# Kernel tuning notes

Hardware: AMD Instinct MI355X
Metric: run time of the kernel (lower is better)

The kernel has to match this reference:

```python
import jax, jax.numpy as jnp
import numpy as np

B, S, D_IN, D_OUT, H = 2, 2048, 1024, 1024, 16
HD = D_OUT // H  # head dim = 64


def setup_inputs() -> dict:
    key = jax.random.key(0)
    ks = jax.random.split(key, 9)
    s_in = 1.0 / np.sqrt(D_IN)
    s_out = 1.0 / np.sqrt(D_OUT)
    return {
        "X": jax.random.normal(ks[0], (B, S, D_IN), dtype=jnp.float32),
        "Wq": jax.random.uniform(ks[1], (D_OUT, D_IN), jnp.float32, -s_in, s_in),
        "bq": jax.random.uniform(ks[2], (D_OUT,), jnp.float32, -s_in, s_in),
        "Wk": jax.random.uniform(ks[3], (D_OUT, D_IN), jnp.float32, -s_in, s_in),
        "bk": jax.random.uniform(ks[4], (D_OUT,), jnp.float32, -s_in, s_in),
        "Wv": jax.random.uniform(ks[5], (D_OUT, D_IN), jnp.float32, -s_in, s_in),
        "bv": jax.random.uniform(ks[6], (D_OUT,), jnp.float32, -s_in, s_in),
        "Wo": jax.random.uniform(ks[7], (D_OUT, D_OUT), jnp.float32, -s_out, s_out),
        "bo": jax.random.uniform(ks[8], (D_OUT,), jnp.float32, -s_out, s_out),
    }


def reference(X, Wq, bq, Wk, bk, Wv, bv, Wo, bo):
    scale = jnp.asarray(HD ** 0.5, X.dtype)  # self.dim = sqrt(head_dim)
    q = X @ Wq.T + bq  # [B,S,D_OUT]
    k = X @ Wk.T + bk
    v = X @ Wv.T + bv
    # split heads: b s (h d) -> b h s d
    q = q.reshape(B, S, H, HD).transpose(0, 2, 1, 3)
    k = k.reshape(B, S, H, HD).transpose(0, 2, 1, 3)
    v = v.reshape(B, S, H, HD).transpose(0, 2, 1, 3)
    scores = jnp.einsum('bhsd,bhtd->bhst', q, k) / scale  # [B,H,S,S]
    causal = jnp.triu(jnp.ones((S, S), dtype=bool), k=1)
    scores = jnp.where(causal, -jnp.inf, scores)
    weights = jax.nn.softmax(scores, axis=-1)
    out = jnp.einsum('bhst,bhtd->bhsd', weights, v)  # [B,H,S,HD]
    out = out.transpose(0, 2, 1, 3).reshape(B, S, D_OUT)  # b h s d -> b s (h d)
    return out @ Wo.T + bo
```

## Files before the change

kernel.cpp:

```cpp
#include <hip/hip_runtime.h>
#include <hip/hip_bf16.h>

typedef __bf16 bf16_t;
typedef __bf16 bf16x8 __attribute__((ext_vector_type(8)));
typedef float  f32x4  __attribute__((ext_vector_type(4)));
typedef unsigned short ushort_t;

#define MFMA16(a, b, c) __builtin_amdgcn_mfma_f32_16x16x32_bf16((a), (b), (c), 0, 0, 0)
#define GLDS16(g, l) __builtin_amdgcn_global_load_lds( \
    (const __attribute__((address_space(1))) unsigned int*)(g), \
    (__attribute__((address_space(3))) unsigned int*)(l), 16, 0, 0)

#define WAITCNT_VM(n)  (0x0F70 | (n))
#define WAITCNT_LGKM0  0xC07F


__global__ __launch_bounds__(64) void sniff_kernel(const ushort_t* __restrict__ x,
                                                   int* __restrict__ flag)
{
    const int t = threadIdx.x;
    const ushort_t u = x[2 * t];
    const int e = (u >> 7) & 0xFF;
    const unsigned long long m = __ballot(e >= 0xA0);
    if (t == 0) *flag = (m != 0ull) ? 1 : 0;
}

__global__ __launch_bounds__(256) void cvt_all(
    const void* __restrict__ X,  const void* __restrict__ W0, const void* __restrict__ W1,
    const void* __restrict__ W2, const void* __restrict__ W3,
    bf16_t* __restrict__ Xb, bf16_t* __restrict__ Wb, const int* __restrict__ flag)
{
    const long long i = (long long)(blockIdx.x * 256 + threadIdx.x) * 8;
    const void* src;
    bf16_t* dst;
    long long off;
    if (i < 4194304) { src = X; dst = Xb; off = i; }
    else {
        const int w = (int)((i - 4194304) >> 20);
        off = (i - 4194304) & 1048575;
        src = (w == 0) ? W0 : (w == 1) ? W1 : (w == 2) ? W2 : W3;
        dst = Wb + (size_t)w * 1048576;
    }
    if (*flag) {
        const float* s = (const float*)src + off;
        const float4 a = *(const float4*)(s);
        const float4 b = *(const float4*)(s + 4);
        bf16x8 o;
        o[0] = (bf16_t)a.x; o[1] = (bf16_t)a.y; o[2] = (bf16_t)a.z; o[3] = (bf16_t)a.w;
        o[4] = (bf16_t)b.x; o[5] = (bf16_t)b.y; o[6] = (bf16_t)b.z; o[7] = (bf16_t)b.w;
        *(bf16x8*)(dst + off) = o;
    } else {
        *(bf16x8*)(dst + off) = *(const bf16x8*)((const bf16_t*)src + off);
    }
}

__global__ __launch_bounds__(256) void cvt_bias(const void* __restrict__ b0, const void* __restrict__ b1,
                                                const void* __restrict__ b2, const void* __restrict__ b3,
                                                float* __restrict__ dst, const int* __restrict__ flag)
{
    const int t = blockIdx.x * 256 + threadIdx.x;
    if (*flag) {
        dst[t]        = ((const float*)b0)[t];
        dst[1024 + t] = ((const float*)b1)[t];
        dst[2048 + t] = ((const float*)b2)[t];
        dst[3072 + t] = ((const float*)b3)[t];
    } else {
        dst[t]        = (float)((const bf16_t*)b0)[t];
        dst[1024 + t] = (float)((const bf16_t*)b1)[t];
        dst[2048 + t] = (float)((const bf16_t*)b2)[t];
        dst[3072 + t] = (float)((const bf16_t*)b3)[t];
    }
}

template<int TM>
__global__ __launch_bounds__(256, 2) void gemm_nt(
    const bf16_t* __restrict__ A,
    const bf16_t* __restrict__ W0, const bf16_t* __restrict__ W1, const bf16_t* __restrict__ W2,
    const float* __restrict__ b0, const float* __restrict__ b1, const float* __restrict__ b2,
    void* __restrict__ C, int ldc, const int* __restrict__ flag, int is_out)
{
    constexpr int MI = TM / 32;
    constexpr int G  = (TM == 128) ? 4 : 3;
    __shared__ bf16_t Ash[3][TM * 32];
    __shared__ bf16_t Bsh[3][128 * 32];

    const int f32out = is_out ? *flag : 0;

    const int tid  = threadIdx.x;
    const int wid  = tid >> 6;
    const int lane = tid & 63;
    const int g    = lane >> 4;
    const int c    = lane & 15;

    const int m0  = blockIdx.x * TM;
    const int n0  = blockIdx.y * 128;
    const int mat = n0 >> 10;
    const bf16_t* W  = (mat == 0) ? W0 : (mat == 1) ? W1 : W2;
    const float*  bs = (mat == 0) ? b0 : (mat == 1) ? b1 : b2;
    const int nw = n0 & 1023;

    const int srow = lane >> 2;
    const int sblk = (lane & 3) ^ ((lane >> 3) & 3);
    const bf16_t* Ag = A + (size_t)(m0 + wid * (TM / 4) + srow) * 1024 + sblk * 8;
    const bf16_t* Wg = W + (size_t)(nw + wid * 32 + srow) * 1024 + sblk * 8;

    const int waveM = (wid >> 1) * (TM / 2);
    const int waveN = (wid & 1) * 64;

    f32x4 acc[MI][4] = {};
    const int fblk = (g ^ ((c >> 1) & 3)) * 8;

    auto stage = [&](int t, int buf) {
        const int k0 = t * 32;
        bf16_t* As = &Ash[buf][(wid * (TM / 4)) * 32];
        bf16_t* Bs = &Bsh[buf][(wid * 32) * 32];
        GLDS16(Ag + k0, As);
        if (TM == 128) GLDS16(Ag + (size_t)16 * 1024 + k0, As + 16 * 32);
        GLDS16(Wg + k0, Bs);
        GLDS16(Wg + (size_t)16 * 1024 + k0, Bs + 16 * 32);
    };

    stage(0, 0);
    stage(1, 1);

    #pragma unroll 3
    for (int k = 0; k < 32; ++k) {
        if (k < 30) {
            stage(k + 2, (k + 2) % 3);
            __builtin_amdgcn_s_waitcnt(WAITCNT_VM(2 * G));
        } else if (k == 30) {
            __builtin_amdgcn_s_waitcnt(WAITCNT_VM(G));
        } else {
            __builtin_amdgcn_s_waitcnt(WAITCNT_VM(0));
        }
        __builtin_amdgcn_s_barrier();
        asm volatile("" ::: "memory");

        const int cur = k % 3;
        bf16x8 af[MI], bfr[4];
        #pragma unroll
        for (int i = 0; i < MI; ++i)
            af[i] = *(const bf16x8*)(&Ash[cur][(waveM + i * 16 + c) * 32 + fblk]);
        #pragma unroll
        for (int j = 0; j < 4; ++j)
            bfr[j] = *(const bf16x8*)(&Bsh[cur][(waveN + j * 16 + c) * 32 + fblk]);
        #pragma unroll
        for (int i = 0; i < MI; ++i)
            #pragma unroll
            for (int j = 0; j < 4; ++j)
                acc[i][j] = MFMA16(af[i], bfr[j], acc[i][j]);

        asm volatile("" ::: "memory");
        __builtin_amdgcn_s_waitcnt(WAITCNT_LGKM0);
        __builtin_amdgcn_s_barrier();
    }

    #pragma unroll
    for (int j = 0; j < 4; ++j) {
        const int col = n0 + waveN + j * 16 + c;
        const float bv = bs[col & 1023];
        #pragma unroll
        for (int i = 0; i < MI; ++i) {
            const int row = m0 + waveM + i * 16 + g * 4;
            #pragma unroll
            for (int r = 0; r < 4; ++r) {
                const float val = acc[i][j][r] + bv;
                const size_t idx = (size_t)(row + r) * ldc + col;
                if (f32out) ((float*)C)[idx] = val;
                else        ((bf16_t*)C)[idx] = (bf16_t)val;
            }
        }
    }
}

__global__ __launch_bounds__(256) void transpose_v(
    const bf16_t* __restrict__ QKV, bf16_t* __restrict__ Vt)
{
    __shared__ ushort_t T[64][72];
    const int tid = threadIdx.x;
    const int r   = tid >> 2;
    const int c0  = (tid & 3) * 16;
    const int bh  = blockIdx.y;
    const int b   = bh >> 4, h = bh & 15;
    const int s0  = blockIdx.x * 64;

    const ushort_t* src = (const ushort_t*)QKV +
        (size_t)(b * 2048 + s0 + r) * 3072 + 2048 + h * 64 + c0;
    ushort_t v[16];
    *(uint4*)(&v[0]) = *(const uint4*)(src);
    *(uint4*)(&v[8]) = *(const uint4*)(src + 8);
    #pragma unroll
    for (int i = 0; i < 16; ++i) T[c0 + i][r] = v[i];
    __syncthreads();
    ushort_t* dst = (ushort_t*)Vt + ((size_t)bh * 64 + r) * 2048 + s0 + c0;
    *(uint4*)(dst)     = *(const uint4*)(&T[r][c0]);
    *(uint4*)(dst + 8) = *(const uint4*)(&T[r][c0 + 8]);
}

__global__ __launch_bounds__(256, 2) void attn_kernel(
    const bf16_t* __restrict__ QKV, const bf16_t* __restrict__ Vt,
    bf16_t* __restrict__ O)
{
    __shared__ bf16_t Ksh[64][72];
    __shared__ bf16_t Vsh[64][72];
    __shared__ bf16_t Psh[4][32][72];

    const int tid  = threadIdx.x;
    const int wid  = tid >> 6;
    const int lane = tid & 63;
    const int g    = lane >> 4;
    const int c    = lane & 15;

    const int bh = blockIdx.y;
    const int b  = bh >> 4, h = bh & 15;
    const int qt = (bh < 16) ? blockIdx.x : (15 - blockIdx.x);
    const int q0 = qt * 128;
    const int nt = 2 * qt + 2;

    bf16x8 aq[2][2];
    #pragma unroll
    for (int qf = 0; qf < 2; ++qf) {
        const bf16_t* qp = QKV + (size_t)(b * 2048 + q0 + wid * 32 + qf * 16 + c) * 3072 + h * 64;
        #pragma unroll
        for (int kb = 0; kb < 2; ++kb) {
            bf16x8 t = *(const bf16x8*)(qp + kb * 32 + g * 8);
            #pragma unroll
            for (int j = 0; j < 8; ++j) t[j] = (bf16_t)((float)t[j] * 0.125f);
            aq[qf][kb] = t;
        }
    }

    float li[2][4] = {};
    f32x4 o[2][4]  = {};

    const int sr  = tid >> 2;
    const int sc0 = (tid & 3) * 16;
    const bf16_t* Kg = QKV + (size_t)(b * 2048 + sr) * 3072 + 1024 + h * 64 + sc0;
    const bf16_t* Vg = Vt + ((size_t)bh * 64 + sr) * 2048 + sc0;

    uint4 kr0 = *(const uint4*)(Kg);
    uint4 kr1 = *(const uint4*)(Kg + 8);
    uint4 vr0 = *(const uint4*)(Vg);
    uint4 vr1 = *(const uint4*)(Vg + 8);

    for (int jt = 0; jt < nt; ++jt) {
        *(uint4*)(&Ksh[sr][sc0])     = kr0;
        *(uint4*)(&Ksh[sr][sc0 + 8]) = kr1;
        *(uint4*)(&Vsh[sr][sc0])     = vr0;
        *(uint4*)(&Vsh[sr][sc0 + 8]) = vr1;
        __syncthreads();

        if (jt + 1 < nt) {
            const size_t ko = (size_t)(jt + 1) * 64 * 3072;
            kr0 = *(const uint4*)(Kg + ko);
            kr1 = *(const uint4*)(Kg + ko + 8);
            vr0 = *(const uint4*)(Vg + (jt + 1) * 64);
            vr1 = *(const uint4*)(Vg + (jt + 1) * 64 + 8);
        }

        f32x4 s[2][4] = {};
        #pragma unroll
        for (int n = 0; n < 4; ++n)
            #pragma unroll
            for (int kb = 0; kb < 2; ++kb) {
                const bf16x8 kf = *(const bf16x8*)(&Ksh[n * 16 + c][kb * 32 + g * 8]);
                s[0][n] = MFMA16(aq[0][kb], kf, s[0][n]);
                s[1][n] = MFMA16(aq[1][kb], kf, s[1][n]);
            }

        if (jt >= nt - 2) {
            const int j0 = jt * 64;
            #pragma unroll
            for (int qf = 0; qf < 2; ++qf) {
                const int qrow = q0 + wid * 32 + qf * 16 + g * 4;
                #pragma unroll
                for (int n = 0; n < 4; ++n)
                    #pragma unroll
                    for (int r = 0; r < 4; ++r)
                        if (j0 + n * 16 + c > qrow + r) s[qf][n][r] = -1e30f;
            }
        }

        #pragma unroll
        for (int qf = 0; qf < 2; ++qf)
            #pragma unroll
            for (int n = 0; n < 4; ++n)
                #pragma unroll
                for (int r = 0; r < 4; ++r) {
                    const float p = __expf(s[qf][n][r]);
                    li[qf][r] += p;
                    Psh[wid][qf * 16 + g * 4 + r][n * 16 + c] = (bf16_t)p;
                }
        __builtin_amdgcn_wave_barrier();

        #pragma unroll
        for (int kb = 0; kb < 2; ++kb) {
            const bf16x8 ap0 = *(const bf16x8*)(&Psh[wid][c][kb * 32 + g * 8]);
            const bf16x8 ap1 = *(const bf16x8*)(&Psh[wid][16 + c][kb * 32 + g * 8]);
            #pragma unroll
            for (int d = 0; d < 4; ++d) {
                const bf16x8 vf = *(const bf16x8*)(&Vsh[d * 16 + c][kb * 32 + g * 8]);
                o[0][d] = MFMA16(ap0, vf, o[0][d]);
                o[1][d] = MFMA16(ap1, vf, o[1][d]);
            }
        }
        __syncthreads();
    }

    #pragma unroll
    for (int off = 1; off < 16; off <<= 1)
        #pragma unroll
        for (int qf = 0; qf < 2; ++qf)
            #pragma unroll
            for (int r = 0; r < 4; ++r)
                li[qf][r] += __shfl_xor(li[qf][r], off, 64);

    #pragma unroll
    for (int qf = 0; qf < 2; ++qf) {
        const int orow = b * 2048 + q0 + wid * 32 + qf * 16 + g * 4;
        #pragma unroll
        for (int r = 0; r < 4; ++r) {
            const float inv = 1.0f / li[qf][r];
            #pragma unroll
            for (int d = 0; d < 4; ++d)
                O[(size_t)(orow + r) * 1024 + h * 64 + d * 16 + c] = (bf16_t)(o[qf][d][r] * inv);
        }
    }
}

extern "C" void kernel_launch(void* const* d_in, const int* in_sizes, int n_in,
                              void* d_out, int out_size, void* d_ws, size_t ws_size,
                              hipStream_t stream)
{
    const void* X  = d_in[0];
    const void* Wq = d_in[1];  const void* bq = d_in[2];
    const void* Wk = d_in[3];  const void* bk = d_in[4];
    const void* Wv = d_in[5];  const void* bv = d_in[6];
    const void* Wo = d_in[7];  const void* bo = d_in[8];

    int*    flag  = (int*)d_ws;
    float*  biasF = (float*)((char*)d_ws + 16);
    bf16_t* Xb    = (bf16_t*)((char*)d_ws + 16 + 16384);
    bf16_t* Wb    = Xb  + (size_t)4096 * 1024;
    bf16_t* QKV   = Wb  + (size_t)4 * 1024 * 1024;
    bf16_t* Vt    = QKV + (size_t)4096 * 3072;
    bf16_t* Ao    = Vt  + (size_t)4096 * 1024;

    const size_t MW = (size_t)1024 * 1024;

    sniff_kernel<<<1, 64, 0, stream>>>((const ushort_t*)X, flag);
    cvt_all<<<4096, 256, 0, stream>>>(X, Wq, Wk, Wv, Wo, Xb, Wb, flag);
    cvt_bias<<<4, 256, 0, stream>>>(bq, bk, bv, bo, biasF, flag);

    gemm_nt<128><<<dim3(32, 24), 256, 0, stream>>>(
        Xb, Wb, Wb + MW, Wb + 2 * MW,
        biasF, biasF + 1024, biasF + 2048, QKV, 3072, flag, 0);
    transpose_v<<<dim3(32, 32), 256, 0, stream>>>(QKV, Vt);
    attn_kernel<<<dim3(16, 32), 256, 0, stream>>>(QKV, Vt, Ao);
    gemm_nt<64><<<dim3(64, 8), 256, 0, stream>>>(
        Ao, Wb + 3 * MW, Wb + 3 * MW, Wb + 3 * MW,
        biasF + 3072, biasF + 3072, biasF + 3072, d_out, 1024, flag, 1);
}
```

Before: 216.8 us.

## Fuse dtype sniff and bias conversion into cvt_all, write V transposed from GEMM

Drops the separate sniff and bias-conversion kernels: every cvt_all block now detects the input dtype itself with a ballot and two extra blocks convert the biases. Removes the transpose_v kernel by having the QKV GEMM write V directly in head-transposed layout from its epilogue. Also switches the QKV GEMM from 128-row to 64-row tiles, which doubles the block count. Together this cuts three launches and a full V round trip through memory, at the cost of strided 8-byte stores in the V epilogue and less reuse per tile in the GEMM.

Measured after the change: 226.1 us. +4.3%, slower.

```diff
diff --git a/kernel.cpp b/kernel.cpp
--- a/kernel.cpp
+++ b/kernel.cpp
@@ -15,22 +15,34 @@
 #define WAITCNT_LGKM0  0xC07F
 
 
-__global__ __launch_bounds__(64) void sniff_kernel(const ushort_t* __restrict__ x,
-                                                   int* __restrict__ flag)
-{
-    const int t = threadIdx.x;
-    const ushort_t u = x[2 * t];
-    const int e = (u >> 7) & 0xFF;
-    const unsigned long long m = __ballot(e >= 0xA0);
-    if (t == 0) *flag = (m != 0ull) ? 1 : 0;
-}
-
 __global__ __launch_bounds__(256) void cvt_all(
     const void* __restrict__ X,  const void* __restrict__ W0, const void* __restrict__ W1,
     const void* __restrict__ W2, const void* __restrict__ W3,
-    bf16_t* __restrict__ Xb, bf16_t* __restrict__ Wb, const int* __restrict__ flag)
+    const void* __restrict__ c0, const void* __restrict__ c1,
+    const void* __restrict__ c2, const void* __restrict__ c3,
+    bf16_t* __restrict__ Xb, bf16_t* __restrict__ Wb, float* __restrict__ biasF,
+    int* __restrict__ flag)
 {
-    const long long i = (long long)(blockIdx.x * 256 + threadIdx.x) * 8;
+    const int tid  = threadIdx.x;
+    const int lane = tid & 63;
+    const ushort_t u = ((const ushort_t*)X)[2 * lane];
+    const int e = (u >> 7) & 0xFF;
+    const int f = (__ballot(e >= 0xA0) != 0ull) ? 1 : 0;
+
+    const int bid = blockIdx.x;
+    if (bid >= 4096) {
+        if (bid == 4096 && tid == 0) *flag = f;
+        const int idx = ((bid - 4096) * 256 + tid) * 8;
+        const int w = idx >> 10, off = idx & 1023;
+        const void* src = (w == 0) ? c0 : (w == 1) ? c1 : (w == 2) ? c2 : c3;
+        #pragma unroll
+        for (int r = 0; r < 8; ++r)
+            biasF[idx + r] = f ? ((const float*)src)[off + r]
+                               : (float)((const bf16_t*)src)[off + r];
+        return;
+    }
+
+    const long long i = (long long)bid * 2048 + tid * 8;
     const void* src;
     bf16_t* dst;
     long long off;
@@ -41,7 +53,7 @@
         src = (w == 0) ? W0 : (w == 1) ? W1 : (w == 2) ? W2 : W3;
         dst = Wb + (size_t)w * 1048576;
     }
-    if (*flag) {
+    if (f) {
         const float* s = (const float*)src + off;
         const float4 a = *(const float4*)(s);
         const float4 b = *(const float4*)(s + 4);
@@ -54,30 +66,13 @@
     }
 }
 
-__global__ __launch_bounds__(256) void cvt_bias(const void* __restrict__ b0, const void* __restrict__ b1,
-                                                const void* __restrict__ b2, const void* __restrict__ b3,
-                                                float* __restrict__ dst, const int* __restrict__ flag)
-{
-    const int t = blockIdx.x * 256 + threadIdx.x;
-    if (*flag) {
-        dst[t]        = ((const float*)b0)[t];
-        dst[1024 + t] = ((const float*)b1)[t];
-        dst[2048 + t] = ((const float*)b2)[t];
-        dst[3072 + t] = ((const float*)b3)[t];
-    } else {
-        dst[t]        = (float)((const bf16_t*)b0)[t];
-        dst[1024 + t] = (float)((const bf16_t*)b1)[t];
-        dst[2048 + t] = (float)((const bf16_t*)b2)[t];
-        dst[3072 + t] = (float)((const bf16_t*)b3)[t];
-    }
-}
-
 template<int TM>
 __global__ __launch_bounds__(256, 2) void gemm_nt(
     const bf16_t* __restrict__ A,
     const bf16_t* __restrict__ W0, const bf16_t* __restrict__ W1, const bf16_t* __restrict__ W2,
     const float* __restrict__ b0, const float* __restrict__ b1, const float* __restrict__ b2,
-    void* __restrict__ C, int ldc, const int* __restrict__ flag, int is_out)
+    void* __restrict__ C, int ldc, bf16_t* __restrict__ Vt, int fuse_vt,
+    const int* __restrict__ flag, int is_out)
 {
     constexpr int MI = TM / 32;
     constexpr int G  = (TM == 128) ? 4 : 3;
@@ -155,6 +150,26 @@
         __builtin_amdgcn_s_barrier();
     }
 
+    if (fuse_vt && mat == 2) {
+        #pragma unroll
+        for (int j = 0; j < 4; ++j) {
+            const int col  = n0 + waveN + j * 16 + c;
+            const int hcol = col & 1023;
+            const float bv = bs[hcol];
+            const int h = hcol >> 6, d = hcol & 63;
+            #pragma unroll
+            for (int i = 0; i < MI; ++i) {
+                const int row = m0 + waveM + i * 16 + g * 4;
+                const int bb = row >> 11, s = row & 2047;
+                bf16_t pk[4];
+                #pragma unroll
+                for (int r = 0; r < 4; ++r) pk[r] = (bf16_t)(acc[i][j][r] + bv);
+                *(uint2*)(&Vt[(((size_t)bb * 16 + h) * 64 + d) * 2048 + s]) = *(uint2*)pk;
+            }
+        }
+        return;
+    }
+
     #pragma unroll
     for (int j = 0; j < 4; ++j) {
         const int col = n0 + waveN + j * 16 + c;
@@ -171,30 +186,6 @@
             }
         }
     }
-}
-
-__global__ __launch_bounds__(256) void transpose_v(
-    const bf16_t* __restrict__ QKV, bf16_t* __restrict__ Vt)
-{
-    __shared__ ushort_t T[64][72];
-    const int tid = threadIdx.x;
-    const int r   = tid >> 2;
-    const int c0  = (tid & 3) * 16;
-    const int bh  = blockIdx.y;
-    const int b   = bh >> 4, h = bh & 15;
-    const int s0  = blockIdx.x * 64;
-
-    const ushort_t* src = (const ushort_t*)QKV +
-        (size_t)(b * 2048 + s0 + r) * 3072 + 2048 + h * 64 + c0;
-    ushort_t v[16];
-    *(uint4*)(&v[0]) = *(const uint4*)(src);
-    *(uint4*)(&v[8]) = *(const uint4*)(src + 8);
-    #pragma unroll
-    for (int i = 0; i < 16; ++i) T[c0 + i][r] = v[i];
-    __syncthreads();
-    ushort_t* dst = (ushort_t*)Vt + ((size_t)bh * 64 + r) * 2048 + s0 + c0;
-    *(uint4*)(dst)     = *(const uint4*)(&T[r][c0]);
-    *(uint4*)(dst + 8) = *(const uint4*)(&T[r][c0 + 8]);
 }
 
 __global__ __launch_bounds__(256, 2) void attn_kernel(
@@ -348,16 +339,14 @@
 
     const size_t MW = (size_t)1024 * 1024;
 
-    sniff_kernel<<<1, 64, 0, stream>>>((const ushort_t*)X, flag);
-    cvt_all<<<4096, 256, 0, stream>>>(X, Wq, Wk, Wv, Wo, Xb, Wb, flag);
-    cvt_bias<<<4, 256, 0, stream>>>(bq, bk, bv, bo, biasF, flag);
-
-    gemm_nt<128><<<dim3(32, 24), 256, 0, stream>>>(
+    cvt_all<<<4098, 256, 0, stream>>>(X, Wq, Wk, Wv, Wo, bq, bk, bv, bo,
+                                      Xb, Wb, biasF, flag);
+
+    gemm_nt<64><<<dim3(64, 24), 256, 0, stream>>>(
         Xb, Wb, Wb + MW, Wb + 2 * MW,
-        biasF, biasF + 1024, biasF + 2048, QKV, 3072, flag, 0);
-    transpose_v<<<dim3(32, 32), 256, 0, stream>>>(QKV, Vt);
+        biasF, biasF + 1024, biasF + 2048, QKV, 3072, Vt, 1, flag, 0);
     attn_kernel<<<dim3(16, 32), 256, 0, stream>>>(QKV, Vt, Ao);
     gemm_nt<64><<<dim3(64, 8), 256, 0, stream>>>(
         Ao, Wb + 3 * MW, Wb + 3 * MW, Wb + 3 * MW,
-        biasF + 3072, biasF + 3072, biasF + 3072, d_out, 1024, flag, 1);
+        biasF + 3072, biasF + 3072, biasF + 3072, d_out, 1024, (bf16_t*)nullptr, 0, flag, 1);
 }
```
